# Optimization experiments

Measured on AMD Instinct MI355X. Metric: run time of the kernel, lower is better.

Reference implementation:

```python
import jax, jax.numpy as jnp
import numpy as np

NUM_HEADS = 8
GROUP = 16
LN_EPS = 1e-5

def _star_relu(x, scale, bias):
    return scale * jnp.square(jax.nn.relu(x)) + bias

def _layernorm(x, w, b):
    mu = x.mean(-1, keepdims=True)
    var = jnp.mean(jnp.square(x - mu), -1, keepdims=True)
    return (x - mu) / jnp.sqrt(var + LN_EPS) * w + b

def _attention(x, qkv_w, proj_w, proj_b, pa_scale, pa_bias, lf_w, lf_b, hf_w, hf_b, lf_gamma, hf_gamma):
    B, N, C = x.shape
    hd = C // NUM_HEADS
    detail = _star_relu(x, pa_scale, pa_bias)
    lf = jnp.tanh(detail @ lf_w.T + lf_b)                      # (B,N,H)
    hf = jax.nn.softplus(detail @ hf_w.T + hf_b)
    hf_sq = jnp.square(hf)
    hf = 2.0 * hf_sq / (hf_sq + 0.3678)
    lf = jnp.repeat(lf, hd, axis=-1)                           # (B,N,C): per-head value repeated across head_dim
    hf = jnp.repeat(hf, hd, axis=-1)
    qkv = (x @ qkv_w.T).reshape(B, N, 3, NUM_HEADS, hd).transpose(2, 0, 3, 1, 4)
    q, k, v = qkv[0], qkv[1], qkv[2]
    q = q * (hd ** -0.5)
    attn = jax.nn.softmax(jnp.einsum('bhqd,bhkd->bhqk', q, k), axis=-1)
    attn_out = jnp.einsum('bhqk,bhkd->bhqd', attn, v).transpose(0, 2, 1, 3).reshape(B, N, C)
    value_tokens = v.transpose(0, 2, 1, 3).reshape(B, N, C)
    high_res = value_tokens - attn_out
    attn_out = attn_out + attn_out * lf * lf_gamma + hf * high_res * hf_gamma
    return attn_out @ proj_w.T + proj_b

def _freq_scale(x, rw1_w, rw1_scale, rw1_bias, rw2_w, freq_w):
    # x: (B,C,H,W); freq_w: (num_filters, C//group, base_size, base_size//2+1) == rfft grid
    B, C, H, W = x.shape
    xf = jnp.fft.rfft2(x, axes=(2, 3), norm='ortho')           # (B,C,fh,fw) complex
    pooled = x.mean(axis=(2, 3))                               # (B,C)
    h = _star_relu(pooled @ rw1_w.T, rw1_scale, rw1_bias)
    routing = jnp.tanh((h @ rw2_w.T).reshape(B, GROUP, -1))    # (B,g,f)
    fh, fw = xf.shape[2], xf.shape[3]
    dyn = jnp.einsum('bgf,fchw->bgchw', routing, freq_w).reshape(B, C, fh, fw)
    xf = xf * dyn
    return jnp.fft.irfft2(xf, s=(H, W), axes=(2, 3), norm='ortho')

def _forward(x, norm1_w, norm1_b, qkv_w, proj_w, proj_b, pa_scale, pa_bias, lf_w, lf_b, hf_w, hf_b,
             lf_gamma, hf_gamma, fs1_rw1_w, fs1_rw1_scale, fs1_rw1_bias, fs1_rw2_w, fs1_fw, gamma_1,
             norm2_w, norm2_b, fc1_w, fc1_b, fc2_w, fc2_b, fs2_rw1_w, fs2_rw1_scale, fs2_rw1_bias,
             fs2_rw2_w, fs2_fw, gamma_2):
    B, C, H, W = x.shape
    tokens = x.reshape(B, C, H * W).transpose(0, 2, 1)         # nchw -> nlc
    att_tokens = _attention(_layernorm(tokens, norm1_w, norm1_b),
                            qkv_w, proj_w, proj_b, pa_scale, pa_bias,
                            lf_w, lf_b, hf_w, hf_b, lf_gamma, hf_gamma)
    att_feat = att_tokens.transpose(0, 2, 1).reshape(B, C, H, W)
    att_feat = _freq_scale(att_feat, fs1_rw1_w, fs1_rw1_scale, fs1_rw1_bias, fs1_rw2_w, fs1_fw) + att_feat
    att_tokens = att_feat.reshape(B, C, H * W).transpose(0, 2, 1)
    tokens = tokens + gamma_1 * att_tokens
    h = _layernorm(tokens, norm2_w, norm2_b)
    mlp_tokens = jax.nn.gelu(h @ fc1_w.T + fc1_b, approximate=False) @ fc2_w.T + fc2_b
    mlp_feat = mlp_tokens.transpose(0, 2, 1).reshape(B, C, H, W)
    mlp_feat = _freq_scale(mlp_feat, fs2_rw1_w, fs2_rw1_scale, fs2_rw1_bias, fs2_rw2_w, fs2_fw) + mlp_feat
    mlp_tokens = mlp_feat.reshape(B, C, H * W).transpose(0, 2, 1)
    tokens = tokens + gamma_2 * mlp_tokens
    return tokens.transpose(0, 2, 1).reshape(B, C, H, W)

def setup_inputs() -> dict:
    key = jax.random.key(0)
    ks = jax.random.split(key, 16)
    B, C, H, W = 16, 512, 32, 32
    heads, group, nf, bs = 8, 16, 4, 32
    hid_rw = int(C * 0.125)
    hid_mlp = int(C * 4.0)
    bfs = bs // 2 + 1
    d = {}
    d['x'] = jax.random.normal(ks[0], (B, C, H, W), jnp.float32)
    d['norm1_w'] = jnp.ones((C,), jnp.float32); d['norm1_b'] = jnp.zeros((C,), jnp.float32)
    d['qkv_w'] = jax.random.normal(ks[1], (3 * C, C), jnp.float32) * 0.02
    d['proj_w'] = jax.random.normal(ks[2], (C, C), jnp.float32) * 0.02
    d['proj_b'] = jnp.zeros((C,), jnp.float32)
    d['pa_scale'] = jnp.ones((1,), jnp.float32); d['pa_bias'] = jnp.zeros((1,), jnp.float32)
    d['lf_w'] = jax.random.normal(ks[3], (heads, C), jnp.float32) * 0.02
    d['lf_b'] = jnp.zeros((heads,), jnp.float32)
    d['hf_w'] = jax.random.normal(ks[4], (heads, C), jnp.float32) * 0.02
    d['hf_b'] = jnp.zeros((heads,), jnp.float32)
    d['lf_gamma'] = 1e-5 * jnp.ones((C,), jnp.float32)
    d['hf_gamma'] = 1e-5 * jnp.ones((C,), jnp.float32)
    d['fs1_rw1_w'] = jax.random.normal(ks[5], (hid_rw, C), jnp.float32) * 0.02
    d['fs1_rw1_scale'] = jnp.ones((1,), jnp.float32); d['fs1_rw1_bias'] = jnp.zeros((1,), jnp.float32)
    d['fs1_rw2_w'] = jax.random.normal(ks[6], (group * nf, hid_rw), jnp.float32) * 0.02
    d['fs1_fw'] = jax.random.normal(ks[7], (nf, C // group, bs, bfs), jnp.float32) * 1e-5
    d['gamma_1'] = 1e-4 * jnp.ones((C,), jnp.float32)
    d['norm2_w'] = jnp.ones((C,), jnp.float32); d['norm2_b'] = jnp.zeros((C,), jnp.float32)
    d['fc1_w'] = jax.random.normal(ks[8], (hid_mlp, C), jnp.float32) * 0.02
    d['fc1_b'] = jnp.zeros((hid_mlp,), jnp.float32)
    d['fc2_w'] = jax.random.normal(ks[9], (C, hid_mlp), jnp.float32) * 0.02
    d['fc2_b'] = jnp.zeros((C,), jnp.float32)
    d['fs2_rw1_w'] = jax.random.normal(ks[10], (hid_rw, C), jnp.float32) * 0.02
    d['fs2_rw1_scale'] = jnp.ones((1,), jnp.float32); d['fs2_rw1_bias'] = jnp.zeros((1,), jnp.float32)
    d['fs2_rw2_w'] = jax.random.normal(ks[11], (group * nf, hid_rw), jnp.float32) * 0.02
    d['fs2_fw'] = jax.random.normal(ks[12], (nf, C // group, bs, bfs), jnp.float32) * 1e-5
    d['gamma_2'] = 1e-4 * jnp.ones((C,), jnp.float32)
    return d

def reference(x, norm1_w, norm1_b, qkv_w, proj_w, proj_b, pa_scale, pa_bias, lf_w, lf_b, hf_w, hf_b,
              lf_gamma, hf_gamma, fs1_rw1_w, fs1_rw1_scale, fs1_rw1_bias, fs1_rw2_w, fs1_fw, gamma_1,
              norm2_w, norm2_b, fc1_w, fc1_b, fc2_w, fc2_b, fs2_rw1_w, fs2_rw1_scale, fs2_rw1_bias,
              fs2_rw2_w, fs2_fw, gamma_2):
    return _forward(x, norm1_w, norm1_b, qkv_w, proj_w, proj_b, pa_scale, pa_bias, lf_w, lf_b, hf_w, hf_b,
                    lf_gamma, hf_gamma, fs1_rw1_w, fs1_rw1_scale, fs1_rw1_bias, fs1_rw2_w, fs1_fw, gamma_1,
                    norm2_w, norm2_b, fc1_w, fc1_b, fc2_w, fc2_b, fs2_rw1_w, fs2_rw1_scale, fs2_rw1_bias,
                    fs2_rw2_w, fs2_fw, gamma_2)
```

## Files before the change

kernel.cpp:

```cpp
#include <hip/hip_runtime.h>
#include <cstdint>
#include <cstddef>

#define B_   16
#define C_   512
#define N_   1024
#define M_   (B_*N_)
#define NH_  8
#define HD_  64
#define C3_  1536
#define CH_  2048

typedef __attribute__((ext_vector_type(8))) short bf16x8;
typedef __attribute__((ext_vector_type(4))) float f32x4;
typedef __attribute__((ext_vector_type(4))) unsigned short u16x4;

__device__ __forceinline__ unsigned short f2bf(float f) {
  union { float f; unsigned u; } v; v.f = f;
  unsigned r = v.u + 0x7fffu + ((v.u >> 16) & 1u);
  return (unsigned short)(r >> 16);
}
__device__ __forceinline__ float bf2f(unsigned short h) {
  union { unsigned u; float f; } v; v.u = ((unsigned)h) << 16;
  return v.f;
}
__device__ __forceinline__ unsigned f2u(float f) {
  union { float f; unsigned u; } v; v.f = f; return v.u;
}

#define GL16(gp, lp) \
  __builtin_amdgcn_global_load_lds( \
      (const __attribute__((address_space(1))) unsigned int*)(const void*)(gp), \
      (__attribute__((address_space(3))) unsigned int*)(void*)(lp), 16, 0, 0)

__global__ __launch_bounds__(256) void k_f2b4(
    const float* __restrict__ s0, unsigned short* __restrict__ d0,
    const float* __restrict__ s1, unsigned short* __restrict__ d1,
    const float* __restrict__ s2, unsigned short* __restrict__ d2,
    const float* __restrict__ s3, unsigned short* __restrict__ d3) {
  int blk = blockIdx.x, t = threadIdx.x;
  const float* s; unsigned short* d; int off;
  if (blk < 3072)      { s = s0; d = d0; off = blk * 256; }
  else if (blk < 4096) { s = s1; d = d1; off = (blk - 3072) * 256; }
  else if (blk < 8192) { s = s2; d = d2; off = (blk - 4096) * 256; }
  else                 { s = s3; d = d3; off = (blk - 8192) * 256; }
  int i = off + t;
  d[i] = f2bf(s[i]);
}

__global__ __launch_bounds__(256) void k_twid(unsigned short* __restrict__ gtab,
                                              float* __restrict__ p1,
                                              float* __restrict__ p2) {
  int idx = blockIdx.x * 256 + threadIdx.x;
  if (idx < 6400) {
    int tab = idx / 1280, rem = idx % 1280;
    int i = rem / 40, j = rem % 40;
    float v = 0.f;
    if (j < 32) {
      float th = 0.19634954084936207f * (float)((i * j) & 31);
      float s, c;
      __sincosf(th, &s, &c);
      if (tab == 0) v = c;
      else if (tab == 1) v = s;
      else if (tab == 2) v = -s;
      else {
        float wg = (j == 0 || j == 16) ? 1.f : 2.f;
        if (j >= 17) wg = 0.f;
        v = (tab == 3) ? wg * c : -wg * s;
      }
    }
    gtab[idx] = f2bf(v);
  } else if (idx < 14592) {
    p1[idx - 6400] = 0.f;
  } else if (idx < 22784) {
    p2[idx - 14592] = 0.f;
  }
}

template<bool WITH>
__global__ __launch_bounds__(256) void k_lnt(const float* __restrict__ src,
    const float* __restrict__ w, const float* __restrict__ bia,
    const float* __restrict__ lfw, const float* __restrict__ lfb,
    const float* __restrict__ hfw, const float* __restrict__ hfb,
    const float* __restrict__ pa_s, const float* __restrict__ pa_b,
    unsigned short* __restrict__ lnout, float* __restrict__ lfout,
    float* __restrict__ hfout) {
  __shared__ unsigned short s[512 * 34];
  const int t = threadIdx.x, wv = t >> 6, l = t & 63;
  const int n0 = blockIdx.x * 32, b = blockIdx.y;
  const int cl = t >> 3;
  const int nn = (t & 7) * 4;
  #pragma unroll
  for (int k = 0; k < 16; ++k) {
    int c = k * 32 + cl;
    float4 v = *(const float4*)&src[(size_t)(b * C_ + c) * N_ + n0 + nn];
    s[c * 34 + nn]     = f2bf(v.x);
    s[c * 34 + nn + 1] = f2bf(v.y);
    s[c * 34 + nn + 2] = f2bf(v.z);
    s[c * 34 + nn + 3] = f2bf(v.w);
  }
  __syncthreads();
  float wv8[8], bv8[8];
  #pragma unroll
  for (int k = 0; k < 8; ++k) { wv8[k] = w[l + 64 * k]; bv8[k] = bia[l + 64 * k]; }
  float ps = 1.f, pb = 0.f;
  if (WITH) { ps = pa_s[0]; pb = pa_b[0]; }
  for (int ri = 0; ri < 8; ++ri) {
    const int n = wv * 8 + ri;
    const int row = b * N_ + n0 + n;
    float v[8];
    #pragma unroll
    for (int k = 0; k < 8; ++k) v[k] = bf2f(s[(l + 64 * k) * 34 + n]);
    float sm = 0.f, q = 0.f;
    #pragma unroll
    for (int k = 0; k < 8; ++k) { sm += v[k]; q += v[k] * v[k]; }
    #pragma unroll
    for (int off = 1; off < 64; off <<= 1) { sm += __shfl_xor(sm, off); q += __shfl_xor(q, off); }
    float mu = sm * (1.f / 512.f);
    float var = q * (1.f / 512.f) - mu * mu;
    float rstd = rsqrtf(var + 1e-5f);
    float ln[8];
    #pragma unroll
    for (int k = 0; k < 8; ++k) ln[k] = (v[k] - mu) * rstd * wv8[k] + bv8[k];
    #pragma unroll
    for (int k = 0; k < 8; ++k)
      lnout[(size_t)row * C_ + l + 64 * k] = f2bf(ln[k]);
    if (WITH) {
      float d[8];
      #pragma unroll
      for (int k = 0; k < 8; ++k) { float r = fmaxf(ln[k], 0.f); d[k] = ps * r * r + pb; }
      float lacc[8], hacc[8];
      #pragma unroll
      for (int h = 0; h < 8; ++h) {
        float la = 0.f, ha = 0.f;
        #pragma unroll
        for (int k = 0; k < 8; ++k) {
          la += d[k] * lfw[h * C_ + l + 64 * k];
          ha += d[k] * hfw[h * C_ + l + 64 * k];
        }
        lacc[h] = la; hacc[h] = ha;
      }
      #pragma unroll
      for (int h = 0; h < 8; ++h)
        #pragma unroll
        for (int off = 1; off < 64; off <<= 1) {
          lacc[h] += __shfl_xor(lacc[h], off);
          hacc[h] += __shfl_xor(hacc[h], off);
        }
      float lv = lacc[0], hv = hacc[0];
      #pragma unroll
      for (int h = 1; h < 8; ++h) { if (l == h) { lv = lacc[h]; hv = hacc[h]; } }
      if (l < 8) {
        lfout[(size_t)row * 8 + l] = tanhf(lv + lfb[l]);
        float z = hv + hfb[l];
        float sp = (z > 15.f) ? z : log1pf(__expf(z));
        float s2 = sp * sp;
        hfout[(size_t)row * 8 + l] = 2.f * s2 / (s2 + 0.3678f);
      }
    }
  }
}

template<int EPI>
__global__ __launch_bounds__(256) void k_gemm(const unsigned short* __restrict__ A,
    const unsigned short* __restrict__ Bt, const float* __restrict__ bias,
    void* __restrict__ outv, unsigned short* __restrict__ vtg, int Nn, int K, int nx) {
  __shared__ __align__(16) unsigned short Asm[2 * 128 * 32];
  __shared__ __align__(16) unsigned short Bsm[2 * 128 * 32];
  const int t = threadIdx.x, w = t >> 6, l = t & 63;
  const int lane15 = l & 15, quad = l >> 4;
  const int cpx = gridDim.x >> 3;
  const int wgs = (blockIdx.x & 7) * cpx + (blockIdx.x >> 3);
  const int bx = wgs % nx, by = wgs / nx;
  const int n0 = bx * 128, m0 = by * 128;
  const int wm = w >> 1, wn = w & 1;
  f32x4 acc[4][4];
  #pragma unroll
  for (int i = 0; i < 4; ++i)
    #pragma unroll
    for (int j = 0; j < 4; ++j) acc[i][j] = (f32x4){0.f, 0.f, 0.f, 0.f};
  const int srow = w * 16 + (l >> 2);
  const int scol = (l & 3) * 8;
  const unsigned short* gA = A + (size_t)(m0 + srow) * K + scol;
  const unsigned short* gB = Bt + (size_t)(n0 + srow) * K + scol;
  const size_t rk64 = (size_t)64 * K;
  auto stage = [&](int bufi, int k0) {
    char* a = (char*)Asm + bufi * 8192 + w * 1024;
    char* bb = (char*)Bsm + bufi * 8192 + w * 1024;
    GL16(gA + k0, a);
    GL16(gA + k0 + rk64, a + 4096);
    GL16(gB + k0, bb);
    GL16(gB + k0 + rk64, bb + 4096);
  };
  stage(0, 0);
  __syncthreads();
  for (int k0 = 0; k0 < K; k0 += 32) {
    const int cur = (k0 >> 5) & 1;
    if (k0 + 32 < K) stage(cur ^ 1, k0 + 32);
    const unsigned short* As = Asm + cur * 4096;
    const unsigned short* Bs = Bsm + cur * 4096;
    bf16x8 af[4], bg[4];
    #pragma unroll
    for (int i = 0; i < 4; ++i)
      af[i] = *(const bf16x8*)&As[(wm * 64 + i * 16 + lane15) * 32 + quad * 8];
    #pragma unroll
    for (int i = 0; i < 4; ++i)
      bg[i] = *(const bf16x8*)&Bs[(wn * 64 + i * 16 + lane15) * 32 + quad * 8];
    #pragma unroll
    for (int i = 0; i < 4; ++i)
      #pragma unroll
      for (int j = 0; j < 4; ++j)
        acc[i][j] = __builtin_amdgcn_mfma_f32_16x16x32_bf16(af[i], bg[j], acc[i][j], 0, 0, 0);
    __syncthreads();
  }
  float psum[4] = {0.f, 0.f, 0.f, 0.f};
  #pragma unroll
  for (int i = 0; i < 4; ++i) {
    int grow = m0 + wm * 64 + i * 16 + quad * 4;
    int bq = grow >> 10, nq = grow & 1023;
    #pragma unroll
    for (int j = 0; j < 4; ++j) {
      int gcol = n0 + wn * 64 + j * 16 + lane15;
      float bs = (EPI == 0) ? 0.f : bias[gcol];
      if (EPI == 1 || EPI == 3) {
        float4 o = make_float4(acc[i][j][0] + bs, acc[i][j][1] + bs,
                               acc[i][j][2] + bs, acc[i][j][3] + bs);
        psum[j] += o.x + o.y + o.z + o.w;
        *(float4*)&((float*)outv)[((size_t)(bq * C_ + gcol) << 10) + nq] = o;
      } else if (EPI == 0) {
        u16x4 pv;
        #pragma unroll
        for (int r = 0; r < 4; ++r) {
          unsigned short hv = f2bf(acc[i][j][r]);
          pv[r] = hv;
          ((unsigned short*)outv)[(size_t)(grow + r) * Nn + gcol] = hv;
        }
        if (gcol >= 1024)
          *(u16x4*)&vtg[((size_t)(bq * C_ + gcol - 1024) << 10) + nq] = pv;
      } else {
        #pragma unroll
        for (int r = 0; r < 4; ++r) {
          float vv = acc[i][j][r] + bs;
          float e = __builtin_amdgcn_exp2f(-(2.302118073f * vv +
                                             0.1029455568f * vv * vv * vv));
          float g = vv * __builtin_amdgcn_rcpf(1.f + e);
          ((unsigned short*)outv)[(size_t)(grow + r) * Nn + gcol] = f2bf(g);
        }
      }
    }
  }
  if (EPI == 1 || EPI == 3) {
    float* pooled = (float*)vtg;
    const int bq = m0 >> 10;
    #pragma unroll
    for (int j = 0; j < 4; ++j) {
      float v = psum[j] * (1.f / 1024.f);
      v += __shfl_xor(v, 16);
      v += __shfl_xor(v, 32);
      if (quad == 0) {
        int gcol = n0 + wn * 64 + j * 16 + lane15;
        atomicAdd(&pooled[bq * C_ + gcol], v);
      }
    }
  }
}

__global__ __launch_bounds__(256, 4) void k_flash(const unsigned short* __restrict__ qkv,
    const unsigned short* __restrict__ vtg, const float* __restrict__ lf,
    const float* __restrict__ hf, const float* __restrict__ lgam,
    const float* __restrict__ hgam, unsigned short* __restrict__ y) {
  const int t = threadIdx.x, w = t >> 6, l = t & 63;
  const int lane15 = l & 15, quad = l >> 4;
  const int wg = (blockIdx.x & 7) * 128 + (blockIdx.x >> 3);
  const int qt = wg & 7;
  const int h = (wg >> 3) & 7;
  const int b = wg >> 6;
  const int q0 = qt * 128;

  __shared__ __align__(16) unsigned short kt[2 * 64 * 64];
  __shared__ __align__(16) unsigned short vt[2 * 64 * 64];
  __shared__ __align__(16) unsigned short pl[4][16 * 64];

  bf16x8 aq[2][2];
  #pragma unroll
  for (int qh = 0; qh < 2; ++qh) {
    const unsigned short* qp = qkv +
        (size_t)(b * N_ + q0 + w * 32 + qh * 16 + lane15) * C3_ + h * 64 + quad * 8;
    bf16x8 r0 = *(const bf16x8*)qp;
    bf16x8 r1 = *(const bf16x8*)(qp + 32);
    #pragma unroll
    for (int i = 0; i < 8; ++i) {
      aq[qh][0][i] = (short)f2bf(0.1803368801111713f * bf2f((unsigned short)r0[i]));
      aq[qh][1][i] = (short)f2bf(0.1803368801111713f * bf2f((unsigned short)r1[i]));
    }
  }
  f32x4 O[2][4];
  #pragma unroll
  for (int qh = 0; qh < 2; ++qh)
    #pragma unroll
    for (int i = 0; i < 4; ++i) O[qh][i] = (f32x4){0.f, 0.f, 0.f, 0.f};
  float lsum[2] = {0.f, 0.f};

  const int prow = w * 8 + (l >> 3);
  const int csw = ((l & 7) ^ (l >> 3)) * 8;
  const unsigned short* kg = qkv + (size_t)(b * N_ + prow) * C3_ + 512 + h * 64 + csw;
  const unsigned short* vg = vtg + (size_t)((b * NH_ + h) * HD_ + prow) * N_ + csw;
  const int swx = (lane15 & 7) * 8;

  auto stage = [&](int bufi, int tile) {
    const unsigned short* kr = kg + (size_t)(tile * 64) * C3_;
    const unsigned short* vr = vg + tile * 64;
    char* kb = (char*)kt + bufi * 8192 + w * 1024;
    char* vb = (char*)vt + bufi * 8192 + w * 1024;
    GL16(kr, kb);
    GL16(kr + (size_t)32 * C3_, kb + 4096);
    GL16(vr, vb);
    GL16(vr + 32 * N_, vb + 4096);
  };

  char* plb = (char*)pl[w] + lane15 * 128;
  const int plx = (lane15 & 7) << 4;

  stage(0, 0);
  __syncthreads();

  for (int kti = 0; kti < 16; ++kti) {
    if (kti < 15) stage((kti + 1) & 1, kti + 1);
    const unsigned short* ktc = kt + (kti & 1) * 4096;
    const unsigned short* vtc = vt + (kti & 1) * 4096;

    #pragma unroll
    for (int qh = 0; qh < 2; ++qh) {
      f32x4 S[4];
      __builtin_amdgcn_s_setprio(1);
      #pragma unroll
      for (int nt = 0; nt < 4; ++nt) {
        const int nrow = nt * 16 + lane15;
        bf16x8 ak0 = *(const bf16x8*)&ktc[nrow * 64 + ((quad * 8) ^ swx)];
        bf16x8 ak1 = *(const bf16x8*)&ktc[nrow * 64 + ((32 + quad * 8) ^ swx)];
        f32x4 z = (f32x4){0.f, 0.f, 0.f, 0.f};
        z = __builtin_amdgcn_mfma_f32_16x16x32_bf16(ak0, aq[qh][0], z, 0, 0, 0);
        z = __builtin_amdgcn_mfma_f32_16x16x32_bf16(ak1, aq[qh][1], z, 0, 0, 0);
        S[nt] = z;
      }
      __builtin_amdgcn_s_setprio(0);
      #pragma unroll
      for (int nt = 0; nt < 4; ++nt)
        #pragma unroll
        for (int r = 0; r < 4; ++r) {
          float pv = __builtin_amdgcn_exp2f(S[nt][r]);
          S[nt][r] = pv;
          lsum[qh] += pv;
        }
      #pragma unroll
      for (int nt = 0; nt < 4; ++nt) {
        unsigned lo = __builtin_amdgcn_perm(f2u(S[nt][1]), f2u(S[nt][0]), 0x07060302u);
        unsigned hi = __builtin_amdgcn_perm(f2u(S[nt][3]), f2u(S[nt][2]), 0x07060302u);
        *(uint2*)(plb + ((nt * 32 + quad * 8) ^ plx)) = make_uint2(lo, hi);
      }
      __builtin_amdgcn_s_setprio(1);
      #pragma unroll
      for (int nc = 0; nc < 2; ++nc) {
        bf16x8 ap = *(const bf16x8*)(plb + ((nc * 64 + quad * 16) ^ plx));
        #pragma unroll
        for (int dt = 0; dt < 4; ++dt) {
          const int vrow = dt * 16 + lane15;
          bf16x8 bv = *(const bf16x8*)&vtc[vrow * 64 + ((nc * 32 + quad * 8) ^ swx)];
          O[qh][dt] = __builtin_amdgcn_mfma_f32_16x16x32_bf16(ap, bv, O[qh][dt], 0, 0, 0);
        }
      }
      __builtin_amdgcn_s_setprio(0);
    }
    __syncthreads();
  }

  #pragma unroll
  for (int qh = 0; qh < 2; ++qh) {
    float s = lsum[qh];
    s += __shfl_xor(s, 16);
    s += __shfl_xor(s, 32);
    float inv = 1.f / s;
    float invr[4], lfr[4], hfr[4];
    const size_t rowb = (size_t)(b * N_ + q0 + w * 32 + qh * 16 + quad * 4);
    #pragma unroll
    for (int r = 0; r < 4; ++r) {
      invr[r] = __shfl(inv, quad * 4 + r);
      lfr[r] = lf[(rowb + r) * 8 + h];
      hfr[r] = hf[(rowb + r) * 8 + h];
    }
    #pragma unroll
    for (int dt = 0; dt < 4; ++dt) {
      const int cc = h * 64 + dt * 16 + lane15;
      const float lg = lgam[cc], hg = hgam[cc];
      #pragma unroll
      for (int r = 0; r < 4; ++r) {
        float a = O[qh][dt][r] * invr[r];
        float vval = bf2f(qkv[(rowb + r) * C3_ + 1024 + cc]);
        float res = a + a * lfr[r] * lg + hfr[r] * (vval - a) * hg;
        y[(rowb + r) * C_ + cc] = f2bf(res);
      }
    }
  }
}

__global__ __launch_bounds__(256) void k_routing(const float* __restrict__ pooled,
    const float* __restrict__ rw1, const float* __restrict__ rw1s,
    const float* __restrict__ rw1b, const float* __restrict__ rw2,
    float* __restrict__ routing) {
  const int b = blockIdx.x, t = threadIdx.x;
  __shared__ float plds[512];
  __shared__ float tile[64][65];
  __shared__ float hl[64];
  plds[t] = pooled[b * 512 + t];
  plds[t + 256] = pooled[b * 512 + t + 256];
  __syncthreads();
  float acc = 0.f;
  for (int c0 = 0; c0 < 512; c0 += 64) {
    #pragma unroll
    for (int kk = 0; kk < 16; ++kk) {
      int idx = kk * 256 + t;
      tile[idx >> 6][idx & 63] = rw1[(size_t)(idx >> 6) * 512 + c0 + (idx & 63)];
    }
    __syncthreads();
    if (t < 64) {
      #pragma unroll
      for (int i = 0; i < 64; ++i) acc += plds[c0 + i] * tile[t][i];
    }
    __syncthreads();
  }
  if (t < 64) {
    float r = fmaxf(acc, 0.f);
    hl[t] = rw1s[0] * r * r + rw1b[0];
  }
  __syncthreads();
  if (t < 64) {
    float r2 = 0.f;
    #pragma unroll
    for (int j = 0; j < 64; ++j) r2 += hl[j] * rw2[(size_t)t * 64 + j];
    routing[b * 64 + t] = tanhf(r2);
  }
}

__global__ __launch_bounds__(256) void k_freq(const float* __restrict__ feat,
    const float* __restrict__ routing, const float* __restrict__ fwtab,
    const unsigned short* __restrict__ gtab, const float* __restrict__ res,
    const float* __restrict__ gamma, float* __restrict__ outp) {
  const int c = blockIdx.x, b = blockIdx.y, t = threadIdx.x;
  const int g = c >> 5, cc = c & 31;
  const int w = t >> 6, l = t & 63;
  const int lane15 = l & 15, quad = l >> 4;
  const int mt = w & 1, nt = w >> 1;
  __shared__ __align__(16) unsigned short Xbf[32 * 40];
  __shared__ __align__(16) float p[32 * 36];
  __shared__ __align__(16) unsigned short Tabs[6400];
  __shared__ __align__(16) unsigned short pl1r[32 * 40], pl1i[32 * 40];
  __shared__ __align__(16) unsigned short pl2r[32 * 40], pl2i[32 * 40];
  __shared__ __align__(16) unsigned short pl3r[32 * 40], pl3i[32 * 40];
  __shared__ float Ms[1024];
  const size_t base = (size_t)(b * C_ + c) * N_;

  {
    float4 v = ((const float4*)(feat + base))[t];
    int hh = t >> 3, w4 = (t & 7) * 4;
    *(float4*)&p[hh * 36 + w4] = v;
    u16x4 xb = { f2bf(v.x), f2bf(v.y), f2bf(v.z), f2bf(v.w) };
    *(u16x4*)&Xbf[hh * 40 + w4] = xb;
  }
  {
    const uint4* src = (const uint4*)gtab;
    uint4* dst = (uint4*)Tabs;
    #pragma unroll
    for (int k = 0; k < 4; ++k) {
      int o = k * 256 + t;
      if (o < 800) dst[o] = src[o];
    }
  }
  {
    float r0 = routing[b * 64 + g * 4 + 0];
    float r1 = routing[b * 64 + g * 4 + 1];
    float r2 = routing[b * 64 + g * 4 + 2];
    float r3 = routing[b * 64 + g * 4 + 3];
    const float* fb = fwtab + (size_t)cc * 544;
    #pragma unroll
    for (int k = 0; k < 4; ++k) {
      int o = k * 256 + t;
      int fh = o >> 5, fw = o & 31;
      float mv = 0.f;
      if (fw < 17) {
        int fi = fh * 17 + fw;
        mv = (r0 * fb[fi] + r1 * fb[17408 + fi] + r2 * fb[34816 + fi] +
              r3 * fb[52224 + fi]) * (1.f / 1024.f);
      }
      Ms[o] = mv;
    }
  }
  __syncthreads();

  const unsigned short* Tc  = Tabs;
  const unsigned short* Ts  = Tabs + 1280;
  const unsigned short* Tsn = Tabs + 2560;
  const unsigned short* Tcw = Tabs + 3840;
  const unsigned short* Tsw = Tabs + 5120;
  const int arow = (mt * 16 + lane15) * 40 + quad * 8;
  const int brow = (nt * 16 + lane15) * 40 + quad * 8;
  const int prow = (nt * 16 + lane15) * 40 + mt * 16 + quad * 4;
  const f32x4 zz = (f32x4){0.f, 0.f, 0.f, 0.f};

  {
    bf16x8 aX = *(const bf16x8*)&Xbf[arow];
    bf16x8 bC = *(const bf16x8*)&Tc[brow];
    bf16x8 bS = *(const bf16x8*)&Tsn[brow];
    f32x4 re = __builtin_amdgcn_mfma_f32_16x16x32_bf16(aX, bC, zz, 0, 0, 0);
    f32x4 im = __builtin_amdgcn_mfma_f32_16x16x32_bf16(aX, bS, zz, 0, 0, 0);
    uint2 pr = make_uint2(__builtin_amdgcn_perm(f2u(re[1]), f2u(re[0]), 0x07060302u),
                          __builtin_amdgcn_perm(f2u(re[3]), f2u(re[2]), 0x07060302u));
    uint2 pi = make_uint2(__builtin_amdgcn_perm(f2u(im[1]), f2u(im[0]), 0x07060302u),
                          __builtin_amdgcn_perm(f2u(im[3]), f2u(im[2]), 0x07060302u));
    *(uint2*)&pl1r[prow] = pr;
    *(uint2*)&pl1i[prow] = pi;
  }
  __syncthreads();
  {
    bf16x8 aC = *(const bf16x8*)&Tc[arow];
    bf16x8 aS = *(const bf16x8*)&Ts[arow];
    bf16x8 aN = *(const bf16x8*)&Tsn[arow];
    bf16x8 bR = *(const bf16x8*)&pl1r[brow];
    bf16x8 bI = *(const bf16x8*)&pl1i[brow];
    f32x4 er = __builtin_amdgcn_mfma_f32_16x16x32_bf16(aC, bR, zz, 0, 0, 0);
    er = __builtin_amdgcn_mfma_f32_16x16x32_bf16(aS, bI, er, 0, 0, 0);
    f32x4 ei = __builtin_amdgcn_mfma_f32_16x16x32_bf16(aC, bI, zz, 0, 0, 0);
    ei = __builtin_amdgcn_mfma_f32_16x16x32_bf16(aN, bR, ei, 0, 0, 0);
    #pragma unroll
    for (int r = 0; r < 4; ++r) {
      float mk = Ms[(mt * 16 + quad * 4 + r) * 32 + nt * 16 + lane15];
      er[r] *= mk; ei[r] *= mk;
    }
    uint2 pr = make_uint2(__builtin_amdgcn_perm(f2u(er[1]), f2u(er[0]), 0x07060302u),
                          __builtin_amdgcn_perm(f2u(er[3]), f2u(er[2]), 0x07060302u));
    uint2 pi = make_uint2(__builtin_amdgcn_perm(f2u(ei[1]), f2u(ei[0]), 0x07060302u),
                          __builtin_amdgcn_perm(f2u(ei[3]), f2u(ei[2]), 0x07060302u));
    *(uint2*)&pl2r[prow] = pr;
    *(uint2*)&pl2i[prow] = pi;
  }
  __syncthreads();
  {
    bf16x8 aR = *(const bf16x8*)&pl2r[arow];
    bf16x8 aI = *(const bf16x8*)&pl2i[arow];
    bf16x8 bC = *(const bf16x8*)&Tc[brow];
    bf16x8 bS = *(const bf16x8*)&Ts[brow];
    bf16x8 bN = *(const bf16x8*)&Tsn[brow];
    f32x4 zr = __builtin_amdgcn_mfma_f32_16x16x32_bf16(aR, bC, zz, 0, 0, 0);
    zr = __builtin_amdgcn_mfma_f32_16x16x32_bf16(aI, bN, zr, 0, 0, 0);
    f32x4 zi = __builtin_amdgcn_mfma_f32_16x16x32_bf16(aI, bC, zz, 0, 0, 0);
    zi = __builtin_amdgcn_mfma_f32_16x16x32_bf16(aR, bS, zi, 0, 0, 0);
    uint2 pr = make_uint2(__builtin_amdgcn_perm(f2u(zr[1]), f2u(zr[0]), 0x07060302u),
                          __builtin_amdgcn_perm(f2u(zr[3]), f2u(zr[2]), 0x07060302u));
    uint2 pi = make_uint2(__builtin_amdgcn_perm(f2u(zi[1]), f2u(zi[0]), 0x07060302u),
                          __builtin_amdgcn_perm(f2u(zi[3]), f2u(zi[2]), 0x07060302u));
    *(uint2*)&pl3r[prow] = pr;
    *(uint2*)&pl3i[prow] = pi;
  }
  __syncthreads();
  {
    bf16x8 aC = *(const bf16x8*)&Tcw[arow];
    bf16x8 aS = *(const bf16x8*)&Tsw[arow];
    bf16x8 bR = *(const bf16x8*)&pl3r[brow];
    bf16x8 bI = *(const bf16x8*)&pl3i[brow];
    f32x4 y = __builtin_amdgcn_mfma_f32_16x16x32_bf16(aC, bR, zz, 0, 0, 0);
    y = __builtin_amdgcn_mfma_f32_16x16x32_bf16(aS, bI, y, 0, 0, 0);
    int hh = nt * 16 + lane15, w0 = mt * 16 + quad * 4;
    float4 fp = *(const float4*)&p[hh * 36 + w0];
    float4 rp = *(const float4*)&res[base + hh * 32 + w0];
    float gv = gamma[c];
    float4 o = make_float4(rp.x + gv * (y[0] + fp.x), rp.y + gv * (y[1] + fp.y),
                           rp.z + gv * (y[2] + fp.z), rp.w + gv * (y[3] + fp.w));
    *(float4*)&outp[base + hh * 32 + w0] = o;
  }
}

extern "C" void kernel_launch(void* const* d_in, const int* in_sizes, int n_in,
                              void* d_out, int out_size, void* d_ws, size_t ws_size,
                              hipStream_t stream) {
  (void)in_sizes; (void)n_in; (void)out_size; (void)ws_size;
  const float* x      = (const float*)d_in[0];
  const float* n1w    = (const float*)d_in[1];
  const float* n1b    = (const float*)d_in[2];
  const float* qkv_w  = (const float*)d_in[3];
  const float* proj_w = (const float*)d_in[4];
  const float* proj_b = (const float*)d_in[5];
  const float* pa_s   = (const float*)d_in[6];
  const float* pa_b   = (const float*)d_in[7];
  const float* lf_w   = (const float*)d_in[8];
  const float* lf_b   = (const float*)d_in[9];
  const float* hf_w   = (const float*)d_in[10];
  const float* hf_b   = (const float*)d_in[11];
  const float* lf_g   = (const float*)d_in[12];
  const float* hf_g   = (const float*)d_in[13];
  const float* f1rw1w = (const float*)d_in[14];
  const float* f1rw1s = (const float*)d_in[15];
  const float* f1rw1b = (const float*)d_in[16];
  const float* f1rw2w = (const float*)d_in[17];
  const float* f1fw   = (const float*)d_in[18];
  const float* gamma1 = (const float*)d_in[19];
  const float* n2w    = (const float*)d_in[20];
  const float* n2b    = (const float*)d_in[21];
  const float* fc1w   = (const float*)d_in[22];
  const float* fc1b   = (const float*)d_in[23];
  const float* fc2w   = (const float*)d_in[24];
  const float* fc2b   = (const float*)d_in[25];
  const float* f2rw1w = (const float*)d_in[26];
  const float* f2rw1s = (const float*)d_in[27];
  const float* f2rw1b = (const float*)d_in[28];
  const float* f2rw2w = (const float*)d_in[29];
  const float* f2fw   = (const float*)d_in[30];
  const float* gamma2 = (const float*)d_in[31];

  char* ws = (char*)d_ws;
  float*          tokens = (float*)(ws + 0);
  float*          f1buf  = (float*)(ws + 33554432ULL);
  float*          f2buf  = (float*)(ws + 67108864ULL);
  unsigned short* regA   = (unsigned short*)(ws + 134217728ULL);
  unsigned short* abuf   = (unsigned short*)(ws + 201326592ULL);
  float*          lfbuf  = (float*)(ws + 218103808ULL);
  float*          hfbuf  = (float*)(ws + 218628096ULL);
  float*          pooled = (float*)(ws + 219152384ULL);
  float*          routing= (float*)(ws + 219185152ULL);
  unsigned short* wq     = (unsigned short*)(ws + 219189248ULL);
  unsigned short* wp     = (unsigned short*)(ws + 220762112ULL);
  unsigned short* w1     = (unsigned short*)(ws + 221286400ULL);
  unsigned short* w2     = (unsigned short*)(ws + 223383552ULL);
  unsigned short* gtab   = (unsigned short*)(ws + 225480704ULL);
  unsigned short* vtg    = (unsigned short*)f1buf;
  float*          pooled2= (float*)(ws + 50331648ULL);

  k_f2b4<<<12288, 256, 0, stream>>>(qkv_w, wq, proj_w, wp, fc1w, w1, fc2w, w2);
  k_twid<<<89, 256, 0, stream>>>(gtab, pooled, pooled2);

  k_lnt<true><<<dim3(32, 16), 256, 0, stream>>>(x, n1w, n1b, lf_w, lf_b, hf_w, hf_b,
                                                pa_s, pa_b, abuf, lfbuf, hfbuf);
  k_gemm<0><<<1536, 256, 0, stream>>>(abuf, wq, n1b, regA, vtg, C3_, C_, 12);
  k_flash<<<1024, 256, 0, stream>>>(regA, vtg, lfbuf, hfbuf, lf_g, hf_g, abuf);
  k_gemm<1><<<512, 256, 0, stream>>>(abuf, wp, proj_b, f2buf,
                                     (unsigned short*)pooled, C_, C_, 4);
  k_routing<<<16, 256, 0, stream>>>(pooled, f1rw1w, f1rw1s, f1rw1b, f1rw2w, routing);
  k_freq<<<dim3(512, 16), 256, 0, stream>>>(f2buf, routing, f1fw, gtab, x, gamma1, tokens);
  k_lnt<false><<<dim3(32, 16), 256, 0, stream>>>(tokens, n2w, n2b, nullptr, nullptr,
                                                 nullptr, nullptr, nullptr, nullptr,
                                                 abuf, nullptr, nullptr);
  k_gemm<2><<<2048, 256, 0, stream>>>(abuf, w1, fc1b, regA, nullptr, CH_, C_, 16);
  k_gemm<3><<<512, 256, 0, stream>>>(regA, w2, fc2b, f2buf,
                                     (unsigned short*)pooled2, C_, CH_, 4);
  k_routing<<<16, 256, 0, stream>>>(pooled2, f2rw1w, f2rw1s, f2rw1b, f2rw2w, routing);
  k_freq<<<dim3(512, 16), 256, 0, stream>>>(f2buf, routing, f2fw, gtab, tokens, gamma2,
                                            (float*)d_out);
}
```

Before: 503.1 us.

## Store GEMM outputs as bf16 for freq kernel; single-buffer flash K/V tiles

```diff
diff --git a/kernel.cpp b/kernel.cpp
--- a/kernel.cpp
+++ b/kernel.cpp
@@ -226,7 +226,8 @@
         float4 o = make_float4(acc[i][j][0] + bs, acc[i][j][1] + bs,
                                acc[i][j][2] + bs, acc[i][j][3] + bs);
         psum[j] += o.x + o.y + o.z + o.w;
-        *(float4*)&((float*)outv)[((size_t)(bq * C_ + gcol) << 10) + nq] = o;
+        u16x4 pv = { f2bf(o.x), f2bf(o.y), f2bf(o.z), f2bf(o.w) };
+        *(u16x4*)&((unsigned short*)outv)[((size_t)(bq * C_ + gcol) << 10) + nq] = pv;
       } else if (EPI == 0) {
         u16x4 pv;
         #pragma unroll
@@ -277,9 +278,9 @@
   const int b = wg >> 6;
   const int q0 = qt * 128;
 
-  __shared__ __align__(16) unsigned short kt[2 * 64 * 64];
-  __shared__ __align__(16) unsigned short vt[2 * 64 * 64];
-  __shared__ __align__(16) unsigned short pl[4][16 * 64];
+  __shared__ __align__(16) unsigned short kt[64 * 64];
+  __shared__ __align__(16) unsigned short vt[64 * 64];
+  __shared__ __align__(16) unsigned short pl[4][16 * 72];
 
   bf16x8 aq[2][2];
   #pragma unroll
@@ -305,29 +306,21 @@
   const int csw = ((l & 7) ^ (l >> 3)) * 8;
   const unsigned short* kg = qkv + (size_t)(b * N_ + prow) * C3_ + 512 + h * 64 + csw;
   const unsigned short* vg = vtg + (size_t)((b * NH_ + h) * HD_ + prow) * N_ + csw;
+  char* ktb0 = (char*)kt + w * 1024;
+  char* ktb1 = (char*)kt + 4096 + w * 1024;
+  char* vtb0 = (char*)vt + w * 1024;
+  char* vtb1 = (char*)vt + 4096 + w * 1024;
   const int swx = (lane15 & 7) * 8;
 
-  auto stage = [&](int bufi, int tile) {
-    const unsigned short* kr = kg + (size_t)(tile * 64) * C3_;
-    const unsigned short* vr = vg + tile * 64;
-    char* kb = (char*)kt + bufi * 8192 + w * 1024;
-    char* vb = (char*)vt + bufi * 8192 + w * 1024;
-    GL16(kr, kb);
-    GL16(kr + (size_t)32 * C3_, kb + 4096);
-    GL16(vr, vb);
-    GL16(vr + 32 * N_, vb + 4096);
-  };
-
-  char* plb = (char*)pl[w] + lane15 * 128;
-  const int plx = (lane15 & 7) << 4;
-
-  stage(0, 0);
-  __syncthreads();
-
   for (int kti = 0; kti < 16; ++kti) {
-    if (kti < 15) stage((kti + 1) & 1, kti + 1);
-    const unsigned short* ktc = kt + (kti & 1) * 4096;
-    const unsigned short* vtc = vt + (kti & 1) * 4096;
+    __syncthreads();
+    const unsigned short* kr = kg + (size_t)(kti * 64) * C3_;
+    GL16(kr, ktb0);
+    GL16(kr + (size_t)32 * C3_, ktb1);
+    const unsigned short* vr = vg + kti * 64;
+    GL16(vr, vtb0);
+    GL16(vr + 32 * N_, vtb1);
+    __syncthreads();
 
     #pragma unroll
     for (int qh = 0; qh < 2; ++qh) {
@@ -336,8 +329,8 @@
       #pragma unroll
       for (int nt = 0; nt < 4; ++nt) {
         const int nrow = nt * 16 + lane15;
-        bf16x8 ak0 = *(const bf16x8*)&ktc[nrow * 64 + ((quad * 8) ^ swx)];
-        bf16x8 ak1 = *(const bf16x8*)&ktc[nrow * 64 + ((32 + quad * 8) ^ swx)];
+        bf16x8 ak0 = *(const bf16x8*)&kt[nrow * 64 + ((quad * 8) ^ swx)];
+        bf16x8 ak1 = *(const bf16x8*)&kt[nrow * 64 + ((32 + quad * 8) ^ swx)];
         f32x4 z = (f32x4){0.f, 0.f, 0.f, 0.f};
         z = __builtin_amdgcn_mfma_f32_16x16x32_bf16(ak0, aq[qh][0], z, 0, 0, 0);
         z = __builtin_amdgcn_mfma_f32_16x16x32_bf16(ak1, aq[qh][1], z, 0, 0, 0);
@@ -356,22 +349,21 @@
       for (int nt = 0; nt < 4; ++nt) {
         unsigned lo = __builtin_amdgcn_perm(f2u(S[nt][1]), f2u(S[nt][0]), 0x07060302u);
         unsigned hi = __builtin_amdgcn_perm(f2u(S[nt][3]), f2u(S[nt][2]), 0x07060302u);
-        *(uint2*)(plb + ((nt * 32 + quad * 8) ^ plx)) = make_uint2(lo, hi);
+        *(uint2*)&pl[w][lane15 * 72 + nt * 16 + quad * 4] = make_uint2(lo, hi);
       }
       __builtin_amdgcn_s_setprio(1);
       #pragma unroll
       for (int nc = 0; nc < 2; ++nc) {
-        bf16x8 ap = *(const bf16x8*)(plb + ((nc * 64 + quad * 16) ^ plx));
+        bf16x8 ap = *(const bf16x8*)&pl[w][lane15 * 72 + nc * 32 + quad * 8];
         #pragma unroll
         for (int dt = 0; dt < 4; ++dt) {
           const int vrow = dt * 16 + lane15;
-          bf16x8 bv = *(const bf16x8*)&vtc[vrow * 64 + ((nc * 32 + quad * 8) ^ swx)];
+          bf16x8 bv = *(const bf16x8*)&vt[vrow * 64 + ((nc * 32 + quad * 8) ^ swx)];
           O[qh][dt] = __builtin_amdgcn_mfma_f32_16x16x32_bf16(ap, bv, O[qh][dt], 0, 0, 0);
         }
       }
       __builtin_amdgcn_s_setprio(0);
     }
-    __syncthreads();
   }
 
   #pragma unroll
@@ -441,7 +433,7 @@
   }
 }
 
-__global__ __launch_bounds__(256) void k_freq(const float* __restrict__ feat,
+__global__ __launch_bounds__(256) void k_freq(const unsigned short* __restrict__ feat,
     const float* __restrict__ routing, const float* __restrict__ fwtab,
     const unsigned short* __restrict__ gtab, const float* __restrict__ res,
     const float* __restrict__ gamma, float* __restrict__ outp) {
@@ -460,10 +452,10 @@
   const size_t base = (size_t)(b * C_ + c) * N_;
 
   {
-    float4 v = ((const float4*)(feat + base))[t];
+    u16x4 xb = *(const u16x4*)&feat[base + t * 4];
+    float4 v = make_float4(bf2f(xb[0]), bf2f(xb[1]), bf2f(xb[2]), bf2f(xb[3]));
     int hh = t >> 3, w4 = (t & 7) * 4;
     *(float4*)&p[hh * 36 + w4] = v;
-    u16x4 xb = { f2bf(v.x), f2bf(v.y), f2bf(v.z), f2bf(v.w) };
     *(u16x4*)&Xbf[hh * 40 + w4] = xb;
   }
   {
@@ -618,7 +610,7 @@
   char* ws = (char*)d_ws;
   float*          tokens = (float*)(ws + 0);
   float*          f1buf  = (float*)(ws + 33554432ULL);
-  float*          f2buf  = (float*)(ws + 67108864ULL);
+  unsigned short* featb  = (unsigned short*)(ws + 67108864ULL);
   unsigned short* regA   = (unsigned short*)(ws + 134217728ULL);
   unsigned short* abuf   = (unsigned short*)(ws + 201326592ULL);
   float*          lfbuf  = (float*)(ws + 218103808ULL);
@@ -640,17 +632,17 @@
                                                 pa_s, pa_b, abuf, lfbuf, hfbuf);
   k_gemm<0><<<1536, 256, 0, stream>>>(abuf, wq, n1b, regA, vtg, C3_, C_, 12);
   k_flash<<<1024, 256, 0, stream>>>(regA, vtg, lfbuf, hfbuf, lf_g, hf_g, abuf);
-  k_gemm<1><<<512, 256, 0, stream>>>(abuf, wp, proj_b, f2buf,
+  k_gemm<1><<<512, 256, 0, stream>>>(abuf, wp, proj_b, featb,
                                      (unsigned short*)pooled, C_, C_, 4);
   k_routing<<<16, 256, 0, stream>>>(pooled, f1rw1w, f1rw1s, f1rw1b, f1rw2w, routing);
-  k_freq<<<dim3(512, 16), 256, 0, stream>>>(f2buf, routing, f1fw, gtab, x, gamma1, tokens);
+  k_freq<<<dim3(512, 16), 256, 0, stream>>>(featb, routing, f1fw, gtab, x, gamma1, tokens);
   k_lnt<false><<<dim3(32, 16), 256, 0, stream>>>(tokens, n2w, n2b, nullptr, nullptr,
                                                  nullptr, nullptr, nullptr, nullptr,
                                                  abuf, nullptr, nullptr);
   k_gemm<2><<<2048, 256, 0, stream>>>(abuf, w1, fc1b, regA, nullptr, CH_, C_, 16);
-  k_gemm<3><<<512, 256, 0, stream>>>(regA, w2, fc2b, f2buf,
+  k_gemm<3><<<512, 256, 0, stream>>>(regA, w2, fc2b, featb,
                                      (unsigned short*)pooled2, C_, CH_, 4);
   k_routing<<<16, 256, 0, stream>>>(pooled2, f2rw1w, f2rw1s, f2rw1b, f2rw2w, routing);
-  k_freq<<<dim3(512, 16), 256, 0, stream>>>(f2buf, routing, f2fw, gtab, tokens, gamma2,
+  k_freq<<<dim3(512, 16), 256, 0, stream>>>(featb, routing, f2fw, gtab, tokens, gamma2,
                                             (float*)d_out);
 }
```

Result: faster. 487.3 us (-3.1%).
